# Kernel tuning notes

Measured on AMD Instinct MI355X. Metric: run time of the kernel, lower is better.

The kernel has to match this reference:

```python
import jax, jax.numpy as jnp
import numpy as np
import math

B, L, HID = 2, 2048, 1024
NH, DH = 16, 64
MASK_VAL = -1000000000.0  # half_precision_flag == False


def setup_inputs() -> dict:
    key = jax.random.key(0)
    ks = jax.random.split(key, 12)
    s = 0.02
    return {
        "queries": jax.random.normal(ks[0], (B, L, HID), jnp.float32),
        "keys": jax.random.normal(ks[1], (B, L, HID), jnp.float32),
        "values": jax.random.normal(ks[2], (B, L, HID), jnp.float32),
        "mask": jax.random.randint(ks[3], (B, L, L), 0, 2, jnp.int32),
        "Wq": jax.random.normal(ks[4], (HID, NH * DH), jnp.float32) * s,
        "bq": jnp.zeros((NH * DH,), jnp.float32),
        "Wk": jax.random.normal(ks[5], (HID, NH * DH), jnp.float32) * s,
        "bk": jnp.zeros((NH * DH,), jnp.float32),
        "Wv": jax.random.normal(ks[6], (HID, NH * DH), jnp.float32) * s,
        "bv": jnp.zeros((NH * DH,), jnp.float32),
        "Wo": jax.random.normal(ks[7], (NH * DH, HID), jnp.float32) * s,
        "bo": jnp.zeros((HID,), jnp.float32),
    }


def reference(queries, keys, values, mask, Wq, bq, Wk, bk, Wv, bv, Wo, bo):
    # Linear projections: (B, L, NH*DH)
    q = queries @ Wq + bq
    k = keys @ Wk + bk
    v = values @ Wv + bv
    # FAITHFUL to original: raw .view(B, NH, -1, DH) without transpose
    q = q.reshape(B, NH, L, DH)
    k = k.reshape(B, NH, L, DH)
    v = v.reshape(B, NH, L, DH)
    # scaled dot-product scores: (B, NH, L, L)
    scores = jnp.einsum("bhqd,bhkd->bhqk", q, k) / math.sqrt(DH)
    scores = jnp.where(mask[:, None, :, :] == 0, MASK_VAL, scores)
    probs = jax.nn.softmax(scores, axis=-1)  # dropout p=0 -> identity
    ctx = jnp.einsum("bhqk,bhkd->bhqd", probs, v)  # (B, NH, L, DH)
    # transpose(1,2) then flatten heads, as in original
    ctx = ctx.transpose(0, 2, 1, 3).reshape(B, L, NH * DH)
    return ctx @ Wo + bo
```

## Files before the change

kernel.cpp:

```cpp
#include <hip/hip_runtime.h>
#include <stdint.h>

typedef __bf16 bf16;
typedef __bf16 bf16x8 __attribute__((ext_vector_type(8)));
typedef __bf16 bf16x4 __attribute__((ext_vector_type(4)));
typedef __bf16 bf16x2 __attribute__((ext_vector_type(2)));
typedef float  f32x4  __attribute__((ext_vector_type(4)));
typedef float  f32x16 __attribute__((ext_vector_type(16)));
typedef short  s16x4  __attribute__((ext_vector_type(4)));
typedef short  s16x8  __attribute__((ext_vector_type(8)));
typedef unsigned int u32x2 __attribute__((ext_vector_type(2)));
typedef unsigned int u32x4 __attribute__((ext_vector_type(4)));
typedef unsigned long long ull;

#define GLOAD16(gptr, lptr)                                                     \
  __builtin_amdgcn_global_load_lds(                                             \
      (const __attribute__((address_space(1))) void*)(gptr),                    \
      (__attribute__((address_space(3))) void*)(lptr), 16, 0, 0)

#define MFMA16(a, b, c) __builtin_amdgcn_mfma_f32_16x16x32_bf16((a), (b), (c), 0, 0, 0)
#define MFMA32(a, b, c) __builtin_amdgcn_mfma_f32_32x32x16_bf16((a), (b), (c), 0, 0, 0)

static constexpr int B_ = 2, L_ = 2048, NH_ = 16, DH_ = 64;
static constexpr float QSCALE = 0.18033688011112042f;

__global__ __launch_bounds__(256) void k_prep(const float* __restrict__ q,
                                              const float* __restrict__ k,
                                              const float* __restrict__ v,
                                              const int* __restrict__ mask,
                                              const float* __restrict__ wq,
                                              const float* __restrict__ wk,
                                              const float* __restrict__ wv,
                                              const float* __restrict__ wo,
                                              bf16* __restrict__ X,
                                              bf16* __restrict__ Wt,
                                              ull* __restrict__ mb) {
  __shared__ float t[32][33];
  const int bid = blockIdx.x, tid = threadIdx.x;
  if (bid < 32768) {
    int tt = bid * 256 + tid;
    ull bal = __ballot(mask[tt] != 0);
    if ((tid & 63) == 0) mb[tt >> 6] = bal;
  } else if (bid < 45056) {
    int u = bid - 32768;
    int z = u >> 12, x = u & 4095;
    const float* in = z == 0 ? q : (z == 1 ? k : v);
    bf16* out = X + (size_t)z * 4194304;
    int i = x * 256 + tid;
    const float4 f = ((const float4*)in)[i];
    bf16x4 o = {(bf16)f.x, (bf16)f.y, (bf16)f.z, (bf16)f.w};
    ((bf16x4*)out)[i] = o;
  } else {
    int u = bid - 45056;
    int z = u >> 10, rem = u & 1023;
    const float* in = z == 0 ? wq : (z == 1 ? wk : (z == 2 ? wv : wo));
    bf16* out = Wt + (size_t)z * 1048576;
    int bx = (rem & 31) * 32, by = (rem >> 5) * 32;
    int x = tid & 31, y = tid >> 5;
#pragma unroll
    for (int r = 0; r < 4; ++r)
      t[y + r * 8][x] = in[(size_t)(by + y + r * 8) * 1024 + bx + x];
    __syncthreads();
#pragma unroll
    for (int r = 0; r < 4; ++r)
      out[(size_t)(bx + y + r * 8) * 1024 + by + x] = (bf16)t[x][y + r * 8];
  }
}

__global__ __launch_bounds__(256) void k_gemm3(const bf16* __restrict__ Xb,
                                               const bf16* __restrict__ Wb,
                                               const float* __restrict__ b0,
                                               const float* __restrict__ b1,
                                               const float* __restrict__ b2,
                                               bf16* __restrict__ Ob) {
  const int z = blockIdx.z;
  const bf16* A  = Xb + (size_t)z * 4194304;
  const bf16* Bt = Wb + (size_t)z * 1048576;
  const float* bias = z == 0 ? b0 : (z == 1 ? b1 : b2);
  bf16* C = Ob + (size_t)z * 4194304;
  const int m0 = blockIdx.y * 128, n0 = blockIdx.x * 128;
  __shared__ __align__(16) bf16 As[128 * 32];
  __shared__ __align__(16) bf16 Bs[128 * 32];
  const int tid = threadIdx.x, lane = tid & 63, w = tid >> 6, quad = lane >> 4, l15 = lane & 15;
  const int wm = (w & 1) * 64, wn = (w >> 1) * 64;
  f32x4 acc[4][4] = {};
  for (int kt = 0; kt < 32; ++kt) {
    const int kk = kt * 32;
#pragma unroll
    for (int i = 0; i < 2; ++i) {
      int s = tid + i * 256;
      int r = s >> 2, c = (s & 3) ^ ((r >> 1) & 3);
      GLOAD16(A + (size_t)(m0 + r) * 1024 + kk + c * 8, As + s * 8);
      GLOAD16(Bt + (size_t)(n0 + r) * 1024 + kk + c * 8, Bs + s * 8);
    }
    __syncthreads();
    bf16x8 af[4], bb[4];
#pragma unroll
    for (int i = 0; i < 4; ++i) {
      int ra = wm + i * 16 + l15, rb = wn + i * 16 + l15;
      af[i] = *(const bf16x8*)(As + (ra * 4 + (quad ^ ((ra >> 1) & 3))) * 8);
      bb[i] = *(const bf16x8*)(Bs + (rb * 4 + (quad ^ ((rb >> 1) & 3))) * 8);
    }
#pragma unroll
    for (int mi = 0; mi < 4; ++mi)
#pragma unroll
      for (int ni = 0; ni < 4; ++ni)
        acc[mi][ni] = MFMA16(af[mi], bb[ni], acc[mi][ni]);
    __syncthreads();
  }
  const float scale = (z == 0) ? QSCALE : 1.0f;
#pragma unroll
  for (int mi = 0; mi < 4; ++mi)
#pragma unroll
    for (int ni = 0; ni < 4; ++ni) {
      int row = m0 + wm + mi * 16 + quad * 4;
      int col = n0 + wn + ni * 16 + l15;
      float bz = bias[col];
      if (z == 2) {
        int b_ = row >> 11, l = row & 2047;
        int hh = l >> 7;
        int i0 = (l & 127) * 16 + (col >> 6);
        int d  = col & 63;
        bf16* dst = C + (size_t)(b_ * 16 + hh) * 131072;
#pragma unroll
        for (int r = 0; r < 4; ++r) {
          int iK = i0 + 16 * r;
          dst[((size_t)(iK >> 2) * 64 + d) * 4 + (iK & 3)] = (bf16)(acc[mi][ni][r] + bz);
        }
      } else {
#pragma unroll
        for (int r = 0; r < 4; ++r)
          C[(size_t)(row + r) * 1024 + col] = (bf16)((acc[mi][ni][r] + bz) * scale);
      }
    }
}

__global__ __launch_bounds__(256) void k_gemmo(const bf16* __restrict__ A,
                                               const bf16* __restrict__ Bt,
                                               const float* __restrict__ bias,
                                               float* __restrict__ C) {
  const int m0 = blockIdx.y * 64, n0 = blockIdx.x * 128;
  __shared__ __align__(16) bf16 As[64 * 32];
  __shared__ __align__(16) bf16 Bs[128 * 32];
  const int tid = threadIdx.x, lane = tid & 63, w = tid >> 6, quad = lane >> 4, l15 = lane & 15;
  const int wn = w * 32;
  f32x4 acc[4][2] = {};
  for (int kt = 0; kt < 32; ++kt) {
    const int kk = kt * 32;
    {
      int r = tid >> 2, c = (tid & 3) ^ ((r >> 1) & 3);
      GLOAD16(A + (size_t)(m0 + r) * 1024 + kk + c * 8, As + tid * 8);
    }
#pragma unroll
    for (int i = 0; i < 2; ++i) {
      int s = tid + i * 256;
      int r = s >> 2, c = (s & 3) ^ ((r >> 1) & 3);
      GLOAD16(Bt + (size_t)(n0 + r) * 1024 + kk + c * 8, Bs + s * 8);
    }
    __syncthreads();
    bf16x8 af[4], bb[2];
#pragma unroll
    for (int i = 0; i < 4; ++i) {
      int ra = i * 16 + l15;
      af[i] = *(const bf16x8*)(As + (ra * 4 + (quad ^ ((ra >> 1) & 3))) * 8);
    }
#pragma unroll
    for (int i = 0; i < 2; ++i) {
      int rb = wn + i * 16 + l15;
      bb[i] = *(const bf16x8*)(Bs + (rb * 4 + (quad ^ ((rb >> 1) & 3))) * 8);
    }
#pragma unroll
    for (int mi = 0; mi < 4; ++mi)
#pragma unroll
      for (int ni = 0; ni < 2; ++ni)
        acc[mi][ni] = MFMA16(af[mi], bb[ni], acc[mi][ni]);
    __syncthreads();
  }
#pragma unroll
  for (int mi = 0; mi < 4; ++mi)
#pragma unroll
    for (int ni = 0; ni < 2; ++ni) {
      int row = m0 + mi * 16 + quad * 4;
      int col = n0 + wn + ni * 16 + l15;
      float bz = bias[col];
#pragma unroll
      for (int r = 0; r < 4; ++r)
        C[(size_t)(row + r) * 1024 + col] = acc[mi][ni][r] + bz;
    }
}

static __device__ __forceinline__ unsigned pack2(float a, float b) {
  bf16x2 t = {(bf16)a, (bf16)b};
  return __builtin_bit_cast(unsigned, t);
}

__global__ __launch_bounds__(512, 4) void k_flash(const bf16* __restrict__ Qp,
                                                  const bf16* __restrict__ Kp,
                                                  const bf16* __restrict__ Vtp,
                                                  const ull* __restrict__ mb,
                                                  bf16* __restrict__ ctx) {
  const int b = blockIdx.z, h = blockIdx.y, q0 = blockIdx.x * 128;
  const size_t HEAD = 131072;
  const bf16* Q  = Qp  + ((size_t)b * NH_ + h) * HEAD;
  const bf16* K  = Kp  + ((size_t)b * NH_ + h) * HEAD;
  const bf16* Vt = Vtp + ((size_t)b * NH_ + h) * HEAD;
  const ull* mrow = mb + (size_t)b * L_ * 32;

  __shared__ __align__(16) unsigned char RAW[36864];
  bf16* Ksb = (bf16*)RAW;
  bf16* Vsb = (bf16*)(RAW + 16384);
  ull*  Msb = (ull*)(RAW + 32768);

  const int tid = threadIdx.x, lane = tid & 63, w = tid >> 6;
  const int hi = lane >> 5, l31 = lane & 31;
  const int kh = w & 1, qq = w >> 1;

  bf16x8 qf[4];
#pragma unroll
  for (int ks = 0; ks < 4; ++ks)
    qf[ks] = *(const bf16x8*)(Q + (size_t)(q0 + qq * 32 + l31) * 64 + ks * 16 + hi * 8);

  {
    int s = tid;
    int key = s >> 3, c = (s & 7) ^ (key & 7);
    GLOAD16(K + (size_t)key * 64 + c * 8, Ksb + s * 8);
    GLOAD16(Vt + (size_t)s * 8, Vsb + s * 8);
  }
  if (w < 2) {
    int r = w * 64 + lane;
    GLOAD16(mrow + (size_t)(q0 + r) * 32, (bf16*)Msb + r * 8);
  }
  __syncthreads();

  f32x16 accO0 = {}, accO1 = {}, accL = {};
  const s16x8 one8s = {0x3F80, 0x3F80, 0x3F80, 0x3F80, 0x3F80, 0x3F80, 0x3F80, 0x3F80};
  const bf16x8 ones8 = __builtin_bit_cast(bf16x8, one8s);

  for (int kt = 0; kt < 32; ++kt) {
    const int cur = kt & 1;
    const bf16* Kc = Ksb + cur * 4096;
    const bf16* Vc = Vsb + cur * 4096;
    if (kt + 1 < 32) {
      const int nxt = cur ^ 1;
      int s = tid;
      int key = s >> 3, c = (s & 7) ^ (key & 7);
      GLOAD16(K + (size_t)((kt + 1) * 64 + key) * 64 + c * 8, Ksb + nxt * 4096 + s * 8);
      GLOAD16(Vt + (size_t)(kt + 1) * 4096 + s * 8, Vsb + nxt * 4096 + s * 8);
      if ((kt & 1) && w < 2) {
        int r = w * 64 + lane;
        GLOAD16(mrow + (size_t)(q0 + r) * 32 + (kt + 1),
                (bf16*)Msb + (((kt + 1) >> 1) & 1) * 1024 + r * 8);
      }
    }

    f32x16 st = {};
    const int key = kh * 32 + l31;
#pragma unroll
    for (int ks = 0; ks < 4; ++ks) {
      bf16x8 kf = *(const bf16x8*)(Kc + (key * 8 + ((ks * 2 + hi) ^ (key & 7))) * 8);
      st = MFMA32(kf, qf[ks], st);
    }

    const ull word = Msb[((kt >> 1) & 1) * 256 + (qq * 32 + l31) * 2 + cur];
    const unsigned w32 = (unsigned)(word >> (kh * 32 + 4 * hi));
#pragma unroll
    for (int r = 0; r < 16; ++r) {
      const int bit = (r >> 2) * 8 + (r & 3);
      st[r] = (w32 >> bit) & 1u ? __builtin_amdgcn_exp2f(st[r]) : 0.f;
    }

    bf16x8 af[2];
#pragma unroll
    for (int ks2 = 0; ks2 < 2; ++ks2) {
      const int bb = ks2 * 8;
      unsigned c0 = pack2(st[bb + 0], st[bb + 1]);
      unsigned c1 = pack2(st[bb + 2], st[bb + 3]);
      unsigned c2 = pack2(st[bb + 4], st[bb + 5]);
      unsigned c3 = pack2(st[bb + 6], st[bb + 7]);
      u32x2 s0 = __builtin_amdgcn_permlane32_swap(c0, c2, false, false);
      u32x2 s1 = __builtin_amdgcn_permlane32_swap(c1, c3, false, false);
      u32x4 a4 = {s0.x, s1.x, s0.y, s1.y};
      af[ks2] = __builtin_bit_cast(bf16x8, a4);
    }

    accL = MFMA32(af[0], ones8, accL);
    accL = MFMA32(af[1], ones8, accL);

#pragma unroll
    for (int ks2 = 0; ks2 < 2; ++ks2) {
      const int vb = ((kh * 32 + ks2 * 16 + hi * 8) >> 2) * 64 + l31;
      s16x4 a0 = *(const s16x4*)(Vc + (size_t)vb * 4);
      s16x4 a1 = *(const s16x4*)(Vc + (size_t)(vb + 64) * 4);
      s16x4 b0 = *(const s16x4*)(Vc + (size_t)(vb + 32) * 4);
      s16x4 b1 = *(const s16x4*)(Vc + (size_t)(vb + 96) * 4);
      bf16x8 v0 = __builtin_bit_cast(bf16x8, __builtin_shufflevector(a0, a1, 0, 1, 2, 3, 4, 5, 6, 7));
      bf16x8 v1 = __builtin_bit_cast(bf16x8, __builtin_shufflevector(b0, b1, 0, 1, 2, 3, 4, 5, 6, 7));
      accO0 = MFMA32(af[ks2], v0, accO0);
      accO1 = MFMA32(af[ks2], v1, accO1);
    }
    __syncthreads();
  }

  float* red  = (float*)RAW;
  float* redL = (float*)(RAW + 32768);
  if (kh == 1) {
#pragma unroll
    for (int r = 0; r < 16; ++r) {
      const int qrel = (r & 3) + 8 * (r >> 2) + 4 * hi;
      red[qq * 2048 + qrel * 64 + l31]      = accO0[r];
      red[qq * 2048 + qrel * 64 + 32 + l31] = accO1[r];
      if (l31 == 0) redL[qq * 32 + qrel] = accL[r];
    }
  }
  __syncthreads();
  if (kh == 0) {
#pragma unroll
    for (int r = 0; r < 16; ++r) {
      const int qrel = (r & 3) + 8 * (r >> 2) + 4 * hi;
      const float ls = accL[r] + redL[qq * 32 + qrel];
      const float rl = 1.0f / ls;
      const float o0 = accO0[r] + red[qq * 2048 + qrel * 64 + l31];
      const float o1 = accO1[r] + red[qq * 2048 + qrel * 64 + 32 + l31];
      const int rowg = q0 + qq * 32 + qrel;
      ctx[((size_t)b * L_ + rowg) * 1024 + h * 64 + l31]      = (bf16)(o0 * rl);
      ctx[((size_t)b * L_ + rowg) * 1024 + h * 64 + 32 + l31] = (bf16)(o1 * rl);
    }
  }
}

extern "C" void kernel_launch(void* const* d_in, const int* in_sizes, int n_in,
                              void* d_out, int out_size, void* d_ws, size_t ws_size,
                              hipStream_t stream) {
  (void)in_sizes; (void)n_in; (void)out_size; (void)ws_size;
  const float* q    = (const float*)d_in[0];
  const float* k    = (const float*)d_in[1];
  const float* v    = (const float*)d_in[2];
  const int*   mask = (const int*)d_in[3];
  const float* Wq = (const float*)d_in[4];
  const float* bq = (const float*)d_in[5];
  const float* Wk = (const float*)d_in[6];
  const float* bk = (const float*)d_in[7];
  const float* Wv = (const float*)d_in[8];
  const float* bv = (const float*)d_in[9];
  const float* Wo = (const float*)d_in[10];
  const float* bo = (const float*)d_in[11];
  float* out = (float*)d_out;

  char* ws = (char*)d_ws;
  const size_t SX = (size_t)4096 * 1024 * 2;
  const size_t SW = (size_t)1024 * 1024 * 2;
  bf16* X   = (bf16*)(ws);
  bf16* Wt  = (bf16*)(ws + 3 * SX);
  bf16* QKV = (bf16*)(ws + 3 * SX + 4 * SW);
  bf16* Qp  = QKV;
  bf16* Kp  = QKV + 4194304;
  bf16* Vtp = QKV + 2 * 4194304;
  bf16* Ctx = (bf16*)(ws + 6 * SX + 4 * SW);
  ull* mbits = (ull*)(ws + 7 * SX + 4 * SW);

  dim3 blk(256);
  k_prep<<<49152, blk, 0, stream>>>(q, k, v, mask, Wq, Wk, Wv, Wo, X, Wt, mbits);

  k_gemm3<<<dim3(8, 32, 3), blk, 0, stream>>>(X, Wt, bq, bk, bv, QKV);

  k_flash<<<dim3(16, NH_, B_), dim3(512), 0, stream>>>(Qp, Kp, Vtp, mbits, Ctx);

  k_gemmo<<<dim3(8, 64), blk, 0, stream>>>(Ctx, Wt + 3 * 1048576, bo, out);
}
```

Measured before the change: 267.8 us.

## Double-buffer GEMM tiles and stream V and mask directly from global in flash

Both projection GEMMs switch to double-buffered LDS tiles, issuing the next K-slice's loads right after the barrier and dropping one barrier per iteration. The V-transposed layout changes to 8-key groups, so the flash kernel can read V fragments straight from global as contiguous 16-byte vectors instead of staging them in LDS. The mask words are also read from global per lane. K is now staged two tiles at a time with one barrier per 128 keys, and s_setprio hints are placed around the MFMA groups. This trades LDS traffic and barriers for more global/L2 reads of V and the mask inside the inner loop, which may add latency that is hard to hide.

New measurement: 280.2 us. 1.05x slower.

```diff
diff --git a/kernel.cpp b/kernel.cpp
--- a/kernel.cpp
+++ b/kernel.cpp
@@ -79,35 +79,44 @@
   const float* bias = z == 0 ? b0 : (z == 1 ? b1 : b2);
   bf16* C = Ob + (size_t)z * 4194304;
   const int m0 = blockIdx.y * 128, n0 = blockIdx.x * 128;
-  __shared__ __align__(16) bf16 As[128 * 32];
-  __shared__ __align__(16) bf16 Bs[128 * 32];
+  __shared__ __align__(16) bf16 As[2 * 128 * 32];
+  __shared__ __align__(16) bf16 Bs[2 * 128 * 32];
   const int tid = threadIdx.x, lane = tid & 63, w = tid >> 6, quad = lane >> 4, l15 = lane & 15;
   const int wm = (w & 1) * 64, wn = (w >> 1) * 64;
   f32x4 acc[4][4] = {};
+
+#define G3STAGE(KT, BUF)                                                        \
+  {                                                                             \
+    const int kk_ = (KT) * 32;                                                  \
+    _Pragma("unroll")                                                           \
+    for (int i_ = 0; i_ < 2; ++i_) {                                            \
+      int s_ = tid + i_ * 256;                                                  \
+      int r_ = s_ >> 2, c_ = (s_ & 3) ^ ((r_ >> 1) & 3);                        \
+      GLOAD16(A + (size_t)(m0 + r_) * 1024 + kk_ + c_ * 8, As + (BUF) * 4096 + s_ * 8);  \
+      GLOAD16(Bt + (size_t)(n0 + r_) * 1024 + kk_ + c_ * 8, Bs + (BUF) * 4096 + s_ * 8); \
+    }                                                                           \
+  }
+
+  G3STAGE(0, 0);
   for (int kt = 0; kt < 32; ++kt) {
-    const int kk = kt * 32;
-#pragma unroll
-    for (int i = 0; i < 2; ++i) {
-      int s = tid + i * 256;
-      int r = s >> 2, c = (s & 3) ^ ((r >> 1) & 3);
-      GLOAD16(A + (size_t)(m0 + r) * 1024 + kk + c * 8, As + s * 8);
-      GLOAD16(Bt + (size_t)(n0 + r) * 1024 + kk + c * 8, Bs + s * 8);
-    }
+    const int cur = kt & 1;
     __syncthreads();
+    if (kt + 1 < 32) G3STAGE(kt + 1, cur ^ 1);
     bf16x8 af[4], bb[4];
 #pragma unroll
     for (int i = 0; i < 4; ++i) {
       int ra = wm + i * 16 + l15, rb = wn + i * 16 + l15;
-      af[i] = *(const bf16x8*)(As + (ra * 4 + (quad ^ ((ra >> 1) & 3))) * 8);
-      bb[i] = *(const bf16x8*)(Bs + (rb * 4 + (quad ^ ((rb >> 1) & 3))) * 8);
+      af[i] = *(const bf16x8*)(As + cur * 4096 + (ra * 4 + (quad ^ ((ra >> 1) & 3))) * 8);
+      bb[i] = *(const bf16x8*)(Bs + cur * 4096 + (rb * 4 + (quad ^ ((rb >> 1) & 3))) * 8);
     }
 #pragma unroll
     for (int mi = 0; mi < 4; ++mi)
 #pragma unroll
       for (int ni = 0; ni < 4; ++ni)
         acc[mi][ni] = MFMA16(af[mi], bb[ni], acc[mi][ni]);
-    __syncthreads();
-  }
+  }
+#undef G3STAGE
+
   const float scale = (z == 0) ? QSCALE : 1.0f;
 #pragma unroll
   for (int mi = 0; mi < 4; ++mi)
@@ -125,7 +134,7 @@
 #pragma unroll
         for (int r = 0; r < 4; ++r) {
           int iK = i0 + 16 * r;
-          dst[((size_t)(iK >> 2) * 64 + d) * 4 + (iK & 3)] = (bf16)(acc[mi][ni][r] + bz);
+          dst[((size_t)(iK >> 3) * 64 + d) * 8 + (iK & 7)] = (bf16)(acc[mi][ni][r] + bz);
         }
       } else {
 #pragma unroll
@@ -140,42 +149,51 @@
                                                const float* __restrict__ bias,
                                                float* __restrict__ C) {
   const int m0 = blockIdx.y * 64, n0 = blockIdx.x * 128;
-  __shared__ __align__(16) bf16 As[64 * 32];
-  __shared__ __align__(16) bf16 Bs[128 * 32];
+  __shared__ __align__(16) bf16 As[2 * 64 * 32];
+  __shared__ __align__(16) bf16 Bs[2 * 128 * 32];
   const int tid = threadIdx.x, lane = tid & 63, w = tid >> 6, quad = lane >> 4, l15 = lane & 15;
   const int wn = w * 32;
   f32x4 acc[4][2] = {};
+
+#define GOSTAGE(KT, BUF)                                                        \
+  {                                                                             \
+    const int kk_ = (KT) * 32;                                                  \
+    {                                                                           \
+      int r_ = tid >> 2, c_ = (tid & 3) ^ ((r_ >> 1) & 3);                      \
+      GLOAD16(A + (size_t)(m0 + r_) * 1024 + kk_ + c_ * 8, As + (BUF) * 2048 + tid * 8); \
+    }                                                                           \
+    _Pragma("unroll")                                                           \
+    for (int i_ = 0; i_ < 2; ++i_) {                                            \
+      int s_ = tid + i_ * 256;                                                  \
+      int r_ = s_ >> 2, c_ = (s_ & 3) ^ ((r_ >> 1) & 3);                        \
+      GLOAD16(Bt + (size_t)(n0 + r_) * 1024 + kk_ + c_ * 8, Bs + (BUF) * 4096 + s_ * 8); \
+    }                                                                           \
+  }
+
+  GOSTAGE(0, 0);
   for (int kt = 0; kt < 32; ++kt) {
-    const int kk = kt * 32;
-    {
-      int r = tid >> 2, c = (tid & 3) ^ ((r >> 1) & 3);
-      GLOAD16(A + (size_t)(m0 + r) * 1024 + kk + c * 8, As + tid * 8);
-    }
-#pragma unroll
-    for (int i = 0; i < 2; ++i) {
-      int s = tid + i * 256;
-      int r = s >> 2, c = (s & 3) ^ ((r >> 1) & 3);
-      GLOAD16(Bt + (size_t)(n0 + r) * 1024 + kk + c * 8, Bs + s * 8);
-    }
+    const int cur = kt & 1;
     __syncthreads();
+    if (kt + 1 < 32) GOSTAGE(kt + 1, cur ^ 1);
     bf16x8 af[4], bb[2];
 #pragma unroll
     for (int i = 0; i < 4; ++i) {
       int ra = i * 16 + l15;
-      af[i] = *(const bf16x8*)(As + (ra * 4 + (quad ^ ((ra >> 1) & 3))) * 8);
+      af[i] = *(const bf16x8*)(As + cur * 2048 + (ra * 4 + (quad ^ ((ra >> 1) & 3))) * 8);
     }
 #pragma unroll
     for (int i = 0; i < 2; ++i) {
       int rb = wn + i * 16 + l15;
-      bb[i] = *(const bf16x8*)(Bs + (rb * 4 + (quad ^ ((rb >> 1) & 3))) * 8);
+      bb[i] = *(const bf16x8*)(Bs + cur * 4096 + (rb * 4 + (quad ^ ((rb >> 1) & 3))) * 8);
     }
 #pragma unroll
     for (int mi = 0; mi < 4; ++mi)
 #pragma unroll
       for (int ni = 0; ni < 2; ++ni)
         acc[mi][ni] = MFMA16(af[mi], bb[ni], acc[mi][ni]);
-    __syncthreads();
-  }
+  }
+#undef GOSTAGE
+
 #pragma unroll
   for (int mi = 0; mi < 4; ++mi)
 #pragma unroll
@@ -192,6 +210,64 @@
 static __device__ __forceinline__ unsigned pack2(float a, float b) {
   bf16x2 t = {(bf16)a, (bf16)b};
   return __builtin_bit_cast(unsigned, t);
+}
+
+static __device__ __forceinline__ void flash_step(
+    const bf16* __restrict__ Kc, const bf16* __restrict__ Vg, ull word,
+    bf16x8 qf0, bf16x8 qf1, bf16x8 qf2, bf16x8 qf3, bf16x8 ones8,
+    int hi, int l31, int kh, int vo0, int vo1, int vo2, int vo3,
+    f32x16& accO0, f32x16& accO1, f32x16& accL) {
+  bf16x8 v0 = *(const bf16x8*)(Vg + vo0);
+  bf16x8 v1 = *(const bf16x8*)(Vg + vo1);
+  bf16x8 v2 = *(const bf16x8*)(Vg + vo2);
+  bf16x8 v3 = *(const bf16x8*)(Vg + vo3);
+
+  const int keyq = kh * 32 + l31;
+  f32x16 st = {};
+  __builtin_amdgcn_s_setprio(1);
+#pragma unroll
+  for (int ks = 0; ks < 4; ++ks) {
+    bf16x8 kf = *(const bf16x8*)(Kc + (keyq * 8 + ((ks * 2 + hi) ^ (keyq & 7))) * 8);
+    bf16x8 qf = ks == 0 ? qf0 : (ks == 1 ? qf1 : (ks == 2 ? qf2 : qf3));
+    st = MFMA32(kf, qf, st);
+  }
+  __builtin_amdgcn_s_setprio(0);
+
+  const unsigned w32 = (unsigned)(word >> (kh * 32 + 4 * hi));
+#pragma unroll
+  for (int r = 0; r < 16; ++r) {
+    const int bit = (r >> 2) * 8 + (r & 3);
+    st[r] = (w32 >> bit) & 1u ? __builtin_amdgcn_exp2f(st[r]) : 0.f;
+  }
+
+  bf16x8 af0, af1;
+  {
+    unsigned c0 = pack2(st[0], st[1]);
+    unsigned c1 = pack2(st[2], st[3]);
+    unsigned c2 = pack2(st[4], st[5]);
+    unsigned c3 = pack2(st[6], st[7]);
+    u32x2 s0 = __builtin_amdgcn_permlane32_swap(c0, c2, false, false);
+    u32x2 s1 = __builtin_amdgcn_permlane32_swap(c1, c3, false, false);
+    u32x4 a4 = {s0.x, s1.x, s0.y, s1.y};
+    af0 = __builtin_bit_cast(bf16x8, a4);
+    c0 = pack2(st[8], st[9]);
+    c1 = pack2(st[10], st[11]);
+    c2 = pack2(st[12], st[13]);
+    c3 = pack2(st[14], st[15]);
+    s0 = __builtin_amdgcn_permlane32_swap(c0, c2, false, false);
+    s1 = __builtin_amdgcn_permlane32_swap(c1, c3, false, false);
+    u32x4 b4 = {s0.x, s1.x, s0.y, s1.y};
+    af1 = __builtin_bit_cast(bf16x8, b4);
+  }
+
+  __builtin_amdgcn_s_setprio(1);
+  accL  = MFMA32(af0, ones8, accL);
+  accL  = MFMA32(af1, ones8, accL);
+  accO0 = MFMA32(af0, v0, accO0);
+  accO1 = MFMA32(af0, v1, accO1);
+  accO0 = MFMA32(af1, v2, accO0);
+  accO1 = MFMA32(af1, v3, accO1);
+  __builtin_amdgcn_s_setprio(0);
 }
 
 __global__ __launch_bounds__(512, 4) void k_flash(const bf16* __restrict__ Qp,
@@ -206,29 +282,31 @@
   const bf16* Vt = Vtp + ((size_t)b * NH_ + h) * HEAD;
   const ull* mrow = mb + (size_t)b * L_ * 32;
 
-  __shared__ __align__(16) unsigned char RAW[36864];
+  __shared__ __align__(16) unsigned char RAW[33280];
   bf16* Ksb = (bf16*)RAW;
-  bf16* Vsb = (bf16*)(RAW + 16384);
-  ull*  Msb = (ull*)(RAW + 32768);
 
   const int tid = threadIdx.x, lane = tid & 63, w = tid >> 6;
   const int hi = lane >> 5, l31 = lane & 31;
   const int kh = w & 1, qq = w >> 1;
-
-  bf16x8 qf[4];
-#pragma unroll
-  for (int ks = 0; ks < 4; ++ks)
-    qf[ks] = *(const bf16x8*)(Q + (size_t)(q0 + qq * 32 + l31) * 64 + ks * 16 + hi * 8);
-
+  const size_t mwbase = (size_t)(q0 + qq * 32 + l31) * 32;
+  const int vo0 = ((kh * 4 + hi) * 64 + l31) * 8;
+  const int vo1 = vo0 + 256;
+  const int vo2 = vo0 + 1024;
+  const int vo3 = vo2 + 256;
+
+  bf16x8 qf0, qf1, qf2, qf3;
   {
-    int s = tid;
-    int key = s >> 3, c = (s & 7) ^ (key & 7);
+    const bf16* qrow = Q + (size_t)(q0 + qq * 32 + l31) * 64 + hi * 8;
+    qf0 = *(const bf16x8*)(qrow);
+    qf1 = *(const bf16x8*)(qrow + 16);
+    qf2 = *(const bf16x8*)(qrow + 32);
+    qf3 = *(const bf16x8*)(qrow + 48);
+  }
+
+  {
+    int s = tid, key = s >> 3, c = (s & 7) ^ (key & 7);
     GLOAD16(K + (size_t)key * 64 + c * 8, Ksb + s * 8);
-    GLOAD16(Vt + (size_t)s * 8, Vsb + s * 8);
-  }
-  if (w < 2) {
-    int r = w * 64 + lane;
-    GLOAD16(mrow + (size_t)(q0 + r) * 32, (bf16*)Msb + r * 8);
+    GLOAD16(K + (size_t)(64 + key) * 64 + c * 8, Ksb + 4096 + s * 8);
   }
   __syncthreads();
 
@@ -236,68 +314,23 @@
   const s16x8 one8s = {0x3F80, 0x3F80, 0x3F80, 0x3F80, 0x3F80, 0x3F80, 0x3F80, 0x3F80};
   const bf16x8 ones8 = __builtin_bit_cast(bf16x8, one8s);
 
-  for (int kt = 0; kt < 32; ++kt) {
-    const int cur = kt & 1;
-    const bf16* Kc = Ksb + cur * 4096;
-    const bf16* Vc = Vsb + cur * 4096;
-    if (kt + 1 < 32) {
-      const int nxt = cur ^ 1;
-      int s = tid;
-      int key = s >> 3, c = (s & 7) ^ (key & 7);
-      GLOAD16(K + (size_t)((kt + 1) * 64 + key) * 64 + c * 8, Ksb + nxt * 4096 + s * 8);
-      GLOAD16(Vt + (size_t)(kt + 1) * 4096 + s * 8, Vsb + nxt * 4096 + s * 8);
-      if ((kt & 1) && w < 2) {
-        int r = w * 64 + lane;
-        GLOAD16(mrow + (size_t)(q0 + r) * 32 + (kt + 1),
-                (bf16*)Msb + (((kt + 1) >> 1) & 1) * 1024 + r * 8);
-      }
-    }
-
-    f32x16 st = {};
-    const int key = kh * 32 + l31;
-#pragma unroll
-    for (int ks = 0; ks < 4; ++ks) {
-      bf16x8 kf = *(const bf16x8*)(Kc + (key * 8 + ((ks * 2 + hi) ^ (key & 7))) * 8);
-      st = MFMA32(kf, qf[ks], st);
-    }
-
-    const ull word = Msb[((kt >> 1) & 1) * 256 + (qq * 32 + l31) * 2 + cur];
-    const unsigned w32 = (unsigned)(word >> (kh * 32 + 4 * hi));
-#pragma unroll
-    for (int r = 0; r < 16; ++r) {
-      const int bit = (r >> 2) * 8 + (r & 3);
-      st[r] = (w32 >> bit) & 1u ? __builtin_amdgcn_exp2f(st[r]) : 0.f;
-    }
-
-    bf16x8 af[2];
-#pragma unroll
-    for (int ks2 = 0; ks2 < 2; ++ks2) {
-      const int bb = ks2 * 8;
-      unsigned c0 = pack2(st[bb + 0], st[bb + 1]);
-      unsigned c1 = pack2(st[bb + 2], st[bb + 3]);
-      unsigned c2 = pack2(st[bb + 4], st[bb + 5]);
-      unsigned c3 = pack2(st[bb + 6], st[bb + 7]);
-      u32x2 s0 = __builtin_amdgcn_permlane32_swap(c0, c2, false, false);
-      u32x2 s1 = __builtin_amdgcn_permlane32_swap(c1, c3, false, false);
-      u32x4 a4 = {s0.x, s1.x, s0.y, s1.y};
-      af[ks2] = __builtin_bit_cast(bf16x8, a4);
-    }
-
-    accL = MFMA32(af[0], ones8, accL);
-    accL = MFMA32(af[1], ones8, accL);
-
-#pragma unroll
-    for (int ks2 = 0; ks2 < 2; ++ks2) {
-      const int vb = ((kh * 32 + ks2 * 16 + hi * 8) >> 2) * 64 + l31;
-      s16x4 a0 = *(const s16x4*)(Vc + (size_t)vb * 4);
-      s16x4 a1 = *(const s16x4*)(Vc + (size_t)(vb + 64) * 4);
-      s16x4 b0 = *(const s16x4*)(Vc + (size_t)(vb + 32) * 4);
-      s16x4 b1 = *(const s16x4*)(Vc + (size_t)(vb + 96) * 4);
-      bf16x8 v0 = __builtin_bit_cast(bf16x8, __builtin_shufflevector(a0, a1, 0, 1, 2, 3, 4, 5, 6, 7));
-      bf16x8 v1 = __builtin_bit_cast(bf16x8, __builtin_shufflevector(b0, b1, 0, 1, 2, 3, 4, 5, 6, 7));
-      accO0 = MFMA32(af[ks2], v0, accO0);
-      accO1 = MFMA32(af[ks2], v1, accO1);
-    }
+  for (int g = 0; g < 16; ++g) {
+    const int cs = (g & 1) * 2;
+    const ull word0 = mrow[mwbase + 2 * g];
+    const ull word1 = mrow[mwbase + 2 * g + 1];
+    if (g + 1 < 16) {
+      int s = tid, key = s >> 3, c = (s & 7) ^ (key & 7);
+      const int ns = cs ^ 2;
+      const size_t row0 = (size_t)(g + 1) * 128;
+      GLOAD16(K + (row0 + key) * 64 + c * 8, Ksb + ns * 4096 + s * 8);
+      GLOAD16(K + (row0 + 64 + key) * 64 + c * 8, Ksb + (ns + 1) * 4096 + s * 8);
+    }
+    flash_step(Ksb + cs * 4096, Vt + (size_t)(2 * g) * 4096, word0,
+               qf0, qf1, qf2, qf3, ones8, hi, l31, kh, vo0, vo1, vo2, vo3,
+               accO0, accO1, accL);
+    flash_step(Ksb + (cs + 1) * 4096, Vt + (size_t)(2 * g + 1) * 4096, word1,
+               qf0, qf1, qf2, qf3, ones8, hi, l31, kh, vo0, vo1, vo2, vo3,
+               accO0, accO1, accL);
     __syncthreads();
   }
 
```

## Deepen flash attention K/V pipeline to four stages with explicit vmcnt barriers

Applied to the files above, without the earlier changes.

Replaces the double-buffered K/V LDS pipeline with a four-slot ring: three tiles are prefetched ahead, and each step waits with s_waitcnt vmcnt plus s_barrier instead of __syncthreads. Mask words now come straight from global memory into registers a few tiles ahead instead of being staged through LDS. The V projection layout changes to 8-element interleaving so each V fragment is a single 16-byte LDS load, and s_setprio hints are placed around the MFMA bursts. LDS use grows to 64KB and launch bounds drop to 2 blocks per CU, trading occupancy for deeper latency hiding.

After: 275.8 us. +3.0%, slower.

```diff
diff --git a/kernel.cpp b/kernel.cpp
--- a/kernel.cpp
+++ b/kernel.cpp
@@ -125,7 +125,7 @@
 #pragma unroll
         for (int r = 0; r < 4; ++r) {
           int iK = i0 + 16 * r;
-          dst[((size_t)(iK >> 2) * 64 + d) * 4 + (iK & 3)] = (bf16)(acc[mi][ni][r] + bz);
+          dst[((size_t)(iK >> 3) * 64 + d) * 8 + (iK & 7)] = (bf16)(acc[mi][ni][r] + bz);
         }
       } else {
 #pragma unroll
@@ -194,7 +194,63 @@
   return __builtin_bit_cast(unsigned, t);
 }
 
-__global__ __launch_bounds__(512, 4) void k_flash(const bf16* __restrict__ Qp,
+static __device__ __forceinline__ void flash_step(
+    const bf16* __restrict__ Kc, const bf16* __restrict__ Vc, ull word,
+    const bf16x8 (&qf)[4], bf16x8 ones8,
+    int hi, int keyq, int vo0, int vo1, int vo2, int vo3,
+    f32x16& accO0, f32x16& accO1, f32x16& accL) {
+  bf16x8 v0 = *(const bf16x8*)(Vc + vo0);
+  bf16x8 v1 = *(const bf16x8*)(Vc + vo1);
+  bf16x8 v2 = *(const bf16x8*)(Vc + vo2);
+  bf16x8 v3 = *(const bf16x8*)(Vc + vo3);
+
+  f32x16 st = {};
+  __builtin_amdgcn_s_setprio(1);
+#pragma unroll
+  for (int ks = 0; ks < 4; ++ks) {
+    bf16x8 kf = *(const bf16x8*)(Kc + (keyq * 8 + ((ks * 2 + hi) ^ (keyq & 7))) * 8);
+    st = MFMA32(kf, qf[ks], st);
+  }
+  __builtin_amdgcn_s_setprio(0);
+
+  const unsigned w32 = (unsigned)(word >> ((keyq & 32) + 4 * hi));
+#pragma unroll
+  for (int r = 0; r < 16; ++r) {
+    const int bit = (r >> 2) * 8 + (r & 3);
+    st[r] = (w32 >> bit) & 1u ? __builtin_amdgcn_exp2f(st[r]) : 0.f;
+  }
+
+  bf16x8 af0, af1;
+  {
+    unsigned c0 = pack2(st[0], st[1]);
+    unsigned c1 = pack2(st[2], st[3]);
+    unsigned c2 = pack2(st[4], st[5]);
+    unsigned c3 = pack2(st[6], st[7]);
+    u32x2 s0 = __builtin_amdgcn_permlane32_swap(c0, c2, false, false);
+    u32x2 s1 = __builtin_amdgcn_permlane32_swap(c1, c3, false, false);
+    u32x4 a4 = {s0.x, s1.x, s0.y, s1.y};
+    af0 = __builtin_bit_cast(bf16x8, a4);
+    c0 = pack2(st[8], st[9]);
+    c1 = pack2(st[10], st[11]);
+    c2 = pack2(st[12], st[13]);
+    c3 = pack2(st[14], st[15]);
+    s0 = __builtin_amdgcn_permlane32_swap(c0, c2, false, false);
+    s1 = __builtin_amdgcn_permlane32_swap(c1, c3, false, false);
+    u32x4 b4 = {s0.x, s1.x, s0.y, s1.y};
+    af1 = __builtin_bit_cast(bf16x8, b4);
+  }
+
+  __builtin_amdgcn_s_setprio(1);
+  accL  = MFMA32(af0, ones8, accL);
+  accL  = MFMA32(af1, ones8, accL);
+  accO0 = MFMA32(af0, v0, accO0);
+  accO1 = MFMA32(af0, v1, accO1);
+  accO0 = MFMA32(af1, v2, accO0);
+  accO1 = MFMA32(af1, v3, accO1);
+  __builtin_amdgcn_s_setprio(0);
+}
+
+__global__ __launch_bounds__(512, 2) void k_flash(const bf16* __restrict__ Qp,
                                                   const bf16* __restrict__ Kp,
                                                   const bf16* __restrict__ Vtp,
                                                   const ull* __restrict__ mb,
@@ -206,100 +262,70 @@
   const bf16* Vt = Vtp + ((size_t)b * NH_ + h) * HEAD;
   const ull* mrow = mb + (size_t)b * L_ * 32;
 
-  __shared__ __align__(16) unsigned char RAW[36864];
+  __shared__ __align__(16) unsigned char RAW[65536];
   bf16* Ksb = (bf16*)RAW;
-  bf16* Vsb = (bf16*)(RAW + 16384);
-  ull*  Msb = (ull*)(RAW + 32768);
+  bf16* Vsb = (bf16*)(RAW + 32768);
 
   const int tid = threadIdx.x, lane = tid & 63, w = tid >> 6;
   const int hi = lane >> 5, l31 = lane & 31;
   const int kh = w & 1, qq = w >> 1;
+  const int keyq = kh * 32 + l31;
+  const size_t mw = (size_t)(q0 + qq * 32 + l31) * 32;
+  const int vo0 = ((kh * 4 + hi) * 64 + l31) * 8;
+  const int vo1 = vo0 + 256;
+  const int vo2 = vo0 + 1024;
+  const int vo3 = vo2 + 256;
 
   bf16x8 qf[4];
-#pragma unroll
-  for (int ks = 0; ks < 4; ++ks)
-    qf[ks] = *(const bf16x8*)(Q + (size_t)(q0 + qq * 32 + l31) * 64 + ks * 16 + hi * 8);
-
   {
-    int s = tid;
-    int key = s >> 3, c = (s & 7) ^ (key & 7);
-    GLOAD16(K + (size_t)key * 64 + c * 8, Ksb + s * 8);
-    GLOAD16(Vt + (size_t)s * 8, Vsb + s * 8);
-  }
-  if (w < 2) {
-    int r = w * 64 + lane;
-    GLOAD16(mrow + (size_t)(q0 + r) * 32, (bf16*)Msb + r * 8);
-  }
-  __syncthreads();
+    const bf16* qrow = Q + (size_t)(q0 + qq * 32 + l31) * 64 + hi * 8;
+    qf[0] = *(const bf16x8*)(qrow);
+    qf[1] = *(const bf16x8*)(qrow + 16);
+    qf[2] = *(const bf16x8*)(qrow + 32);
+    qf[3] = *(const bf16x8*)(qrow + 48);
+  }
+
+  ull wa = mrow[mw + 0], wb2 = mrow[mw + 1], wc = mrow[mw + 2], wd;
+
+#define STAGE(T, SL)                                                            \
+  {                                                                             \
+    int s_ = tid, key_ = s_ >> 3, c_ = (s_ & 7) ^ (key_ & 7);                   \
+    GLOAD16(K + ((size_t)(T) * 64 + key_) * 64 + c_ * 8, Ksb + (SL) * 4096 + s_ * 8); \
+    GLOAD16(Vt + (size_t)(T) * 4096 + s_ * 8, Vsb + (SL) * 4096 + s_ * 8);      \
+  }
+#define WB(N) asm volatile("s_waitcnt vmcnt(" #N ")\n\ts_barrier" ::: "memory")
+#define STEP(SL, WORD)                                                          \
+  flash_step(Ksb + (SL) * 4096, Vsb + (SL) * 4096, (WORD), qf, ones8, hi, keyq, \
+             vo0, vo1, vo2, vo3, accO0, accO1, accL)
+
+  STAGE(0, 0);
+  STAGE(1, 1);
+  STAGE(2, 2);
 
   f32x16 accO0 = {}, accO1 = {}, accL = {};
   const s16x8 one8s = {0x3F80, 0x3F80, 0x3F80, 0x3F80, 0x3F80, 0x3F80, 0x3F80, 0x3F80};
   const bf16x8 ones8 = __builtin_bit_cast(bf16x8, one8s);
 
-  for (int kt = 0; kt < 32; ++kt) {
-    const int cur = kt & 1;
-    const bf16* Kc = Ksb + cur * 4096;
-    const bf16* Vc = Vsb + cur * 4096;
-    if (kt + 1 < 32) {
-      const int nxt = cur ^ 1;
-      int s = tid;
-      int key = s >> 3, c = (s & 7) ^ (key & 7);
-      GLOAD16(K + (size_t)((kt + 1) * 64 + key) * 64 + c * 8, Ksb + nxt * 4096 + s * 8);
-      GLOAD16(Vt + (size_t)(kt + 1) * 4096 + s * 8, Vsb + nxt * 4096 + s * 8);
-      if ((kt & 1) && w < 2) {
-        int r = w * 64 + lane;
-        GLOAD16(mrow + (size_t)(q0 + r) * 32 + (kt + 1),
-                (bf16*)Msb + (((kt + 1) >> 1) & 1) * 1024 + r * 8);
-      }
-    }
-
-    f32x16 st = {};
-    const int key = kh * 32 + l31;
-#pragma unroll
-    for (int ks = 0; ks < 4; ++ks) {
-      bf16x8 kf = *(const bf16x8*)(Kc + (key * 8 + ((ks * 2 + hi) ^ (key & 7))) * 8);
-      st = MFMA32(kf, qf[ks], st);
-    }
-
-    const ull word = Msb[((kt >> 1) & 1) * 256 + (qq * 32 + l31) * 2 + cur];
-    const unsigned w32 = (unsigned)(word >> (kh * 32 + 4 * hi));
-#pragma unroll
-    for (int r = 0; r < 16; ++r) {
-      const int bit = (r >> 2) * 8 + (r & 3);
-      st[r] = (w32 >> bit) & 1u ? __builtin_amdgcn_exp2f(st[r]) : 0.f;
-    }
-
-    bf16x8 af[2];
-#pragma unroll
-    for (int ks2 = 0; ks2 < 2; ++ks2) {
-      const int bb = ks2 * 8;
-      unsigned c0 = pack2(st[bb + 0], st[bb + 1]);
-      unsigned c1 = pack2(st[bb + 2], st[bb + 3]);
-      unsigned c2 = pack2(st[bb + 4], st[bb + 5]);
-      unsigned c3 = pack2(st[bb + 6], st[bb + 7]);
-      u32x2 s0 = __builtin_amdgcn_permlane32_swap(c0, c2, false, false);
-      u32x2 s1 = __builtin_amdgcn_permlane32_swap(c1, c3, false, false);
-      u32x4 a4 = {s0.x, s1.x, s0.y, s1.y};
-      af[ks2] = __builtin_bit_cast(bf16x8, a4);
-    }
-
-    accL = MFMA32(af[0], ones8, accL);
-    accL = MFMA32(af[1], ones8, accL);
-
-#pragma unroll
-    for (int ks2 = 0; ks2 < 2; ++ks2) {
-      const int vb = ((kh * 32 + ks2 * 16 + hi * 8) >> 2) * 64 + l31;
-      s16x4 a0 = *(const s16x4*)(Vc + (size_t)vb * 4);
-      s16x4 a1 = *(const s16x4*)(Vc + (size_t)(vb + 64) * 4);
-      s16x4 b0 = *(const s16x4*)(Vc + (size_t)(vb + 32) * 4);
-      s16x4 b1 = *(const s16x4*)(Vc + (size_t)(vb + 96) * 4);
-      bf16x8 v0 = __builtin_bit_cast(bf16x8, __builtin_shufflevector(a0, a1, 0, 1, 2, 3, 4, 5, 6, 7));
-      bf16x8 v1 = __builtin_bit_cast(bf16x8, __builtin_shufflevector(b0, b1, 0, 1, 2, 3, 4, 5, 6, 7));
-      accO0 = MFMA32(af[ks2], v0, accO0);
-      accO1 = MFMA32(af[ks2], v1, accO1);
-    }
-    __syncthreads();
-  }
+  WB(4); wd  = mrow[mw + 3]; STAGE(3, 3); STEP(0, wa);
+  WB(5); wa  = mrow[mw + 4]; STAGE(4, 0); STEP(1, wb2);
+  WB(6); wb2 = mrow[mw + 5]; STAGE(5, 1); STEP(2, wc);
+  WB(6); wc  = mrow[mw + 6]; STAGE(6, 2); STEP(3, wd);
+  for (int g = 1; g < 7; ++g) {
+    const int kt0 = g * 4;
+    WB(6); wd  = mrow[mw + kt0 + 3]; STAGE(kt0 + 3, 3); STEP(0, wa);
+    WB(6); wa  = mrow[mw + kt0 + 4]; STAGE(kt0 + 4, 0); STEP(1, wb2);
+    WB(6); wb2 = mrow[mw + kt0 + 5]; STAGE(kt0 + 5, 1); STEP(2, wc);
+    WB(6); wc  = mrow[mw + kt0 + 6]; STAGE(kt0 + 6, 2); STEP(3, wd);
+  }
+  WB(6); wd = mrow[mw + 31]; STAGE(31, 3); STEP(0, wa);
+  WB(5); STEP(1, wb2);
+  WB(3); STEP(2, wc);
+  WB(0); STEP(3, wd);
+#undef STEP
+#undef WB
+#undef STAGE
+
+  __syncthreads();
 
   float* red  = (float*)RAW;
   float* redL = (float*)(RAW + 32768);
```
